# Kernel tuning notes

Hardware: AMD Instinct MI355X
Metric: run time of the kernel (lower is better)

## Reference

```python
import jax, jax.numpy as jnp
import numpy as np

B, P, V = 32, 32, 200          # batch, minPockets, vertices per pocket
NF, NT, NR, NROT = 4, 16, 5, 16
TR = NT * NR                   # 80 kernel bins
MAX_RHO = 12.0
NLIG = 7
TWO_PI = 2.0 * np.pi


def _initial_polar_grid():
    grid_rho = np.linspace(0.0, MAX_RHO, NR + 1)[1:]
    grid_theta = np.linspace(0.0, TWO_PI, NT + 1)[:-1]
    gr, gt = np.meshgrid(grid_rho, grid_theta)
    return gr.T.flatten().astype(np.float32), gt.T.flatten().astype(np.float32)


def _glorot(k, shape):
    lim = np.sqrt(6.0 / (shape[-2] + shape[-1]))
    return jax.random.uniform(k, shape, jnp.float32, -lim, lim)


def setup_inputs() -> dict:
    key = jax.random.key(0)
    ks = jax.random.split(key, 8)
    input_feat = jax.random.normal(ks[0], (B, P, V, NF), jnp.float32)
    rho_coords = jax.random.uniform(ks[1], (B, P, V, 1), jnp.float32) * MAX_RHO
    theta_coords = jax.random.uniform(ks[2], (B, P, V, 1), jnp.float32) * TWO_PI
    mask = jnp.ones((B, P, V, 1), jnp.float32)
    gr, gt = _initial_polar_grid()
    mu_rho = jnp.tile(jnp.asarray(gr)[None], (NF, 1))        # [F,TR]
    mu_theta = jnp.tile(jnp.asarray(gt)[None], (NF, 1))      # [F,TR]
    sigma_rho = jnp.full((NF, TR), MAX_RHO / 8.0, jnp.float32)
    sigma_theta = jnp.ones((NF, TR), jnp.float32)
    W_conv = _glorot(ks[3], (NF, TR, TR))
    b_conv = jnp.zeros((NF, TR), jnp.float32)
    W1 = _glorot(ks[4], (NF * TR, TR)); b1 = jnp.zeros((TR,), jnp.float32)
    W2 = _glorot(ks[5], (TR * TR, 64)); b2 = jnp.zeros((64,), jnp.float32)
    W3 = _glorot(ks[6], (64, NLIG));    b3 = jnp.zeros((NLIG,), jnp.float32)
    bn = lambda d: (jnp.ones((d,), jnp.float32), jnp.zeros((d,), jnp.float32),
                    jnp.zeros((d,), jnp.float32), jnp.ones((d,), jnp.float32))
    bn1_g, bn1_b, bn1_m, bn1_v = bn(NF * TR)
    bn2_g, bn2_b, bn2_m, bn2_v = bn(TR)
    bn3_g, bn3_b, bn3_m, bn3_v = bn(64)
    return dict(input_feat=input_feat, rho_coords=rho_coords, theta_coords=theta_coords,
                mask=mask, mu_rho=mu_rho, sigma_rho=sigma_rho, mu_theta=mu_theta,
                sigma_theta=sigma_theta, W_conv=W_conv, b_conv=b_conv, W1=W1, b1=b1,
                bn1_g=bn1_g, bn1_b=bn1_b, bn1_m=bn1_m, bn1_v=bn1_v,
                bn2_g=bn2_g, bn2_b=bn2_b, bn2_m=bn2_m, bn2_v=bn2_v,
                W2=W2, b2=b2, bn3_g=bn3_g, bn3_b=bn3_b, bn3_m=bn3_m, bn3_v=bn3_v,
                W3=W3, b3=b3)


def _bn(x, g, b, m, v, eps=1e-3):
    return (x - m) * (g * jax.lax.rsqrt(v + eps)) + b


def _conv_layer(input_feat, rho, theta, mask, mu_rho, sigma_rho, mu_theta, sigma_theta,
                W_conv, b_conv, eps=1e-5):
    # rho/theta/mask: [B,P,V,1]; mu/sigma: [F,TR]; feat: [B,P,V,F]
    # rho Gaussian is rotation-invariant -> compute once.  [B,P,V,F,TR]
    rho_g = jnp.exp(-jnp.square(rho[..., None] - mu_rho) / (jnp.square(sigma_rho) + eps))
    offs = (TWO_PI / NROT) * jnp.arange(NROT, dtype=jnp.float32)

    def step(best, off):
        th = jnp.mod(theta + off, TWO_PI)
        th_g = jnp.exp(-jnp.square(th[..., None] - mu_theta) / (jnp.square(sigma_theta) + eps))
        g = rho_g * th_g * mask[..., None]                      # [B,P,V,F,TR]
        g = g / (jnp.sum(g, axis=2, keepdims=True) + eps)       # normalize over vertices
        desc = jnp.einsum('bpvft,bpvf->bpft', g, input_feat)    # [B,P,F,TR]
        conv = jnp.einsum('bpft,ftu->bpfu', desc, W_conv) + b_conv
        return jnp.maximum(best, conv), None

    init = jnp.full((B, P, NF, TR), -jnp.inf, jnp.float32)
    best, _ = jax.lax.scan(step, init, offs)
    return best                                                  # [B,P,F,TR]


def reference(input_feat, rho_coords, theta_coords, mask, mu_rho, sigma_rho, mu_theta,
              sigma_theta, W_conv, b_conv, W1, b1, bn1_g, bn1_b, bn1_m, bn1_v,
              bn2_g, bn2_b, bn2_m, bn2_v, W2, b2, bn3_g, bn3_b, bn3_m, bn3_v, W3, b3):
    conv = _conv_layer(input_feat, rho_coords, theta_coords, mask, mu_rho, sigma_rho,
                       mu_theta, sigma_theta, W_conv, b_conv)
    x = conv.reshape(B, P, NF * TR)
    x = jax.nn.relu(_bn(x, bn1_g, bn1_b, bn1_m, bn1_v))
    x = x @ W1 + b1                                              # [B,P,TR]
    x = jax.nn.relu(_bn(x, bn2_g, bn2_b, bn2_m, bn2_v))
    cov = jnp.einsum('bpi,bpj->bij', x, x) / jnp.float32(P)      # CovarLayer [B,TR,TR]
    x = cov.reshape(B, TR * TR)
    x = jax.nn.relu(x @ W2 + b2)                                 # Dense(64, relu)
    x = _bn(x, bn3_g, bn3_b, bn3_m, bn3_v)
    return x @ W3 + b3                                           # [B, NLIG]
```

## Files before the change

### kernel.cpp

```cpp
#include <hip/hip_runtime.h>
#include <math.h>

#define B_    32
#define P_    32
#define V_    200
#define NF_   4
#define TR_   80
#define NROT_ 16
#define NLIG_ 7
#define NTH_  1024
#define PKT_  512

#define WSLOTS 33
#define CSTR   (WSLOTS * 25)
#define CTOT   (16 * CSTR)
#define RSTR   84

static constexpr float TWO_PI_F  = 6.2831854820251465f;
static constexpr float DELTA_F   = 0.39269909262657166f;

__global__ __launch_bounds__(NTH_, 4) void masif_conv_kernel(
    const float* __restrict__ feat, const float* __restrict__ rho,
    const float* __restrict__ theta, const float* __restrict__ mask,
    const float* __restrict__ mu_rho, const float* __restrict__ sigma_rho,
    const float* __restrict__ mu_theta, const float* __restrict__ sigma_theta,
    const float* __restrict__ W_conv, const float* __restrict__ b_conv,
    const float* __restrict__ W1, const float* __restrict__ b1,
    const float* __restrict__ bn1_g, const float* __restrict__ bn1_b,
    const float* __restrict__ bn1_m, const float* __restrict__ bn1_v,
    const float* __restrict__ bn2_g, const float* __restrict__ bn2_b,
    const float* __restrict__ bn2_m, const float* __restrict__ bn2_v,
    float* __restrict__ x2out)
{
    __shared__ __align__(16) float s_C[2][CTOT];
    __shared__ __align__(16) float s_V[2][V_][12];
    __shared__ float s_offs[NROT_];
    __shared__ float s_mu[5], s_isr[5];
    __shared__ float s_ist1;
    __shared__ int   s_cnt[2][16], s_start[2][17];
    __shared__ int   s_whist[2][4][16];

    const int tid = threadIdx.x;
    const int pk  = tid >> 9;
    const int lt  = tid & 511;
    const int bp  = blockIdx.x * 2 + pk;
    const size_t vb = (size_t)bp * V_;

    float* Cp = s_C[pk];

    float*  stg_th  = Cp;
    float*  stg_rho = Cp + 256;
    float*  stg_msk = Cp + 512;
    float4* stg_f4  = (float4*)(Cp + 768);

    for (int i = lt; i < V_; i += PKT_) {
        stg_th[i]  = theta[vb + i];
        stg_rho[i] = rho[vb + i];
        stg_msk[i] = mask[vb + i];
        stg_f4[i]  = ((const float4*)(feat + vb * NF_))[i];
    }
    if (tid < NROT_) s_offs[tid] = (float)tid * DELTA_F;
    if (tid < 5) {
        s_mu[tid] = mu_rho[tid * 16];
        float sg = sigma_rho[tid * 16];
        s_isr[tid] = 1.0f / (sg * sg + 1e-5f);
    }
    if (tid == 5) { float sg = sigma_theta[0]; s_ist1 = 1.0f / (sg * sg + 1e-5f); }
    if (tid >= 64 && tid < 96) ((int*)s_cnt)[tid - 64] = 0;
    __syncthreads();

    int myb = 0;
    if (lt < V_) {
        float th = stg_th[lt];
        int rs = 16;
        for (int r = 1; r < 16; ++r) {
            if (th + s_offs[r] >= TWO_PI_F) { rs = r; break; }
        }
        myb = rs - 1;
        atomicAdd(&s_cnt[pk][myb], 1);
    }

    int rkw = 0;
    {
        const unsigned long long below = (1ULL << (tid & 63)) - 1ULL;
        const int wv = lt >> 6;
        for (int b = 0; b < 16; ++b) {
            bool p = (lt < V_) && (myb == b);
            unsigned long long m = __ballot(p);
            if (p) rkw = __popcll(m & below);
            if (wv < 4 && (tid & 63) == b) s_whist[pk][wv][b] = __popcll(m);
        }
    }
    __syncthreads();
    if (lt == 0) {
        int run = 0;
        for (int k = 0; k < 16; ++k) { s_start[pk][k] = run; run += s_cnt[pk][k]; }
        s_start[pk][16] = run;
    }
    __syncthreads();

    if (lt < V_) {
        int rk = rkw;
        for (int w = 0; w < (lt >> 6); ++w) rk += s_whist[pk][w][myb];
        int pos = s_start[pk][myb] + rk;
        float th = stg_th[lt];
        float mk = stg_msk[lt];
        float4 f4 = stg_f4[lt];
        float rv = stg_rho[lt];
        float R[5];
        #pragma unroll
        for (int i = 0; i < 5; ++i) {
            float d = rv - s_mu[i];
            R[i] = __expf(-d * d * s_isr[i]);
        }
        *(float4*)&s_V[pk][pos][0] = make_float4(R[0], R[1], R[2], R[3]);
        *(float4*)&s_V[pk][pos][4] = make_float4(R[4], th, f4.x * mk, f4.y * mk);
        *(float4*)&s_V[pk][pos][8] = make_float4(f4.z * mk, f4.w * mk, mk, 0.0f);
    }
    __syncthreads();

    {
        float4 z4 = make_float4(0.f, 0.f, 0.f, 0.f);
        float4* C4 = (float4*)Cp;
        for (int e = lt; e < CTOT / 4; e += PKT_) C4[e] = z4;
    }
    __syncthreads();

    {
        const int team = lt >> 5, t32 = lt & 31;
        const int cg = t32 / 6;
        const int mq = t32 - cg * 6;
        const float ist = s_ist1;
        float acc[4][5];
        #pragma unroll
        for (int mm = 0; mm < 4; ++mm)
            #pragma unroll
            for (int i = 0; i < 5; ++i) acc[mm][i] = 0.0f;
        const int v0 = s_start[pk][team], v1 = s_start[pk][team + 1];
        const float nbase = (float)(team - 25 + mq * 4);
        if (cg < 5) {
            for (int v = v0; v < v1; ++v) {
                float4 ra = *(const float4*)&s_V[pk][v][0];
                const float r4 = s_V[pk][v][4];
                const float th = s_V[pk][v][5];
                const float ch = s_V[pk][v][6 + cg];
                float A0 = ch * ra.x, A1 = ch * ra.y, A2 = ch * ra.z,
                      A3 = ch * ra.w, A4 = ch * r4;
                #pragma unroll
                for (int mm = 0; mm < 4; ++mm) {
                    float q = fmaf(nbase + (float)mm, DELTA_F, th);
                    float w = __expf(-q * q * ist);
                    acc[mm][0] = fmaf(w, A0, acc[mm][0]);
                    acc[mm][1] = fmaf(w, A1, acc[mm][1]);
                    acc[mm][2] = fmaf(w, A2, acc[mm][2]);
                    acc[mm][3] = fmaf(w, A3, acc[mm][3]);
                    acc[mm][4] = fmaf(w, A4, acc[mm][4]);
                }
            }
            #pragma unroll
            for (int mm = 0; mm < 4; ++mm) {
                const int l = mq * 4 + mm;
                const int w = team - 1 + l;
                if (l < 20 && w >= 0 && w < WSLOTS)
                    #pragma unroll
                    for (int i = 0; i < 5; ++i)
                        Cp[team * CSTR + w * 25 + cg * 5 + i] = acc[mm][i];
            }
        }
    }
    __syncthreads();

    for (int e = lt; e < CSTR; e += PKT_) {
        float run = Cp[e];
        #pragma unroll
        for (int tk = 1; tk < 16; ++tk) {
            run += Cp[tk * CSTR + e];
            Cp[tk * CSTR + e] = run;
        }
    }
    __syncthreads();

    const float* Tb = Cp + 15 * CSTR;
    float dreg[10];
    #pragma unroll
    for (int it = 0; it < 10; ++it) {
        const int q   = lt + PKT_ * it;
        const int r   = q / 320;
        const int bin = q - r * 320;
        const int j1 = bin & 15, ci1 = bin >> 4;
        const int i1 = ci1 % 5;
        const int sD = ci1, sS = 20 + i1;
        const int wT = r - j1 + 24;
        const bool pT = (wT <= 32);
        const int wTc = pT ? wT : 32;
        const float* Tp = Tb + wTc * 25;
        float tD = Tp[sD], tS = Tp[sS];
        float D = pT ? tD : 0.0f;
        float S = pT ? tS : 0.0f;
        if (r > 0) {
            const float* Cr = Cp + (r - 1) * CSTR;
            const float* Up = Cr + wTc * 25;
            float uD = Up[sD], uS = Up[sS];
            if (pT) { D -= uD; S -= uS; }
            const int wW = wT - 16;
            const bool pW = (wW >= 0);
            const int wWc = pW ? wW : 0;
            const float* Wp = Cr + wWc * 25;
            float wD = Wp[sD], wS = Wp[sS];
            if (pW) { D += wD; S += wS; }
        }
        dreg[it] = D / (S + 1e-5f);
    }
    __syncthreads();

    float* ring    = Cp;
    float* s_pool2 = Cp + 5376;
    float* s_x1    = Cp + 6656;
    float* s_part  = Cp + 6976;

    #pragma unroll
    for (int it = 0; it < 10; ++it) {
        const int q   = lt + PKT_ * it;
        const int r   = q / 320;
        const int bin = q - r * 320;
        const int j1 = bin & 15, ci1 = bin >> 4;
        const int c1 = ci1 / 5, i1 = ci1 - c1 * 5;
        ring[r * (4 * RSTR) + c1 * RSTR + i1 * 16 + j1] = dreg[it];
    }
    __syncthreads();

    if (lt < 320) {
        const int g  = lt / 80;
        const int s  = lt - g * 80;
        const int cf = s / 20;
        const int uq = s - cf * 20;
        const int u0 = uq * 4;
        const float* Wf = W_conv + (size_t)cf * TR_ * TR_ + u0;
        const float* r0 = ring + (4 * g) * (4 * RSTR) + cf * RSTR;
        float4 a0 = make_float4(0.f, 0.f, 0.f, 0.f);
        float4 a1 = a0, a2 = a0, a3 = a0;
        #pragma unroll 4
        for (int kq = 0; kq < 20; ++kq) {
            const int k = kq * 4;
            float4 d0 = *(const float4*)&r0[k];
            float4 d1 = *(const float4*)&r0[(4 * RSTR) + k];
            float4 d2 = *(const float4*)&r0[(8 * RSTR) + k];
            float4 d3 = *(const float4*)&r0[(12 * RSTR) + k];
            float4 w0 = *(const float4*)&Wf[(size_t)(k + 0) * TR_];
            float4 w1 = *(const float4*)&Wf[(size_t)(k + 1) * TR_];
            float4 w2 = *(const float4*)&Wf[(size_t)(k + 2) * TR_];
            float4 w3 = *(const float4*)&Wf[(size_t)(k + 3) * TR_];
            a0.x = fmaf(d0.x,w0.x, fmaf(d0.y,w1.x, fmaf(d0.z,w2.x, fmaf(d0.w,w3.x, a0.x))));
            a0.y = fmaf(d0.x,w0.y, fmaf(d0.y,w1.y, fmaf(d0.z,w2.y, fmaf(d0.w,w3.y, a0.y))));
            a0.z = fmaf(d0.x,w0.z, fmaf(d0.y,w1.z, fmaf(d0.z,w2.z, fmaf(d0.w,w3.z, a0.z))));
            a0.w = fmaf(d0.x,w0.w, fmaf(d0.y,w1.w, fmaf(d0.z,w2.w, fmaf(d0.w,w3.w, a0.w))));
            a1.x = fmaf(d1.x,w0.x, fmaf(d1.y,w1.x, fmaf(d1.z,w2.x, fmaf(d1.w,w3.x, a1.x))));
            a1.y = fmaf(d1.x,w0.y, fmaf(d1.y,w1.y, fmaf(d1.z,w2.y, fmaf(d1.w,w3.y, a1.y))));
            a1.z = fmaf(d1.x,w0.z, fmaf(d1.y,w1.z, fmaf(d1.z,w2.z, fmaf(d1.w,w3.z, a1.z))));
            a1.w = fmaf(d1.x,w0.w, fmaf(d1.y,w1.w, fmaf(d1.z,w2.w, fmaf(d1.w,w3.w, a1.w))));
            a2.x = fmaf(d2.x,w0.x, fmaf(d2.y,w1.x, fmaf(d2.z,w2.x, fmaf(d2.w,w3.x, a2.x))));
            a2.y = fmaf(d2.x,w0.y, fmaf(d2.y,w1.y, fmaf(d2.z,w2.y, fmaf(d2.w,w3.y, a2.y))));
            a2.z = fmaf(d2.x,w0.z, fmaf(d2.y,w1.z, fmaf(d2.z,w2.z, fmaf(d2.w,w3.z, a2.z))));
            a2.w = fmaf(d2.x,w0.w, fmaf(d2.y,w1.w, fmaf(d2.z,w2.w, fmaf(d2.w,w3.w, a2.w))));
            a3.x = fmaf(d3.x,w0.x, fmaf(d3.y,w1.x, fmaf(d3.z,w2.x, fmaf(d3.w,w3.x, a3.x))));
            a3.y = fmaf(d3.x,w0.y, fmaf(d3.y,w1.y, fmaf(d3.z,w2.y, fmaf(d3.w,w3.y, a3.y))));
            a3.z = fmaf(d3.x,w0.z, fmaf(d3.y,w1.z, fmaf(d3.z,w2.z, fmaf(d3.w,w3.z, a3.z))));
            a3.w = fmaf(d3.x,w0.w, fmaf(d3.y,w1.w, fmaf(d3.z,w2.w, fmaf(d3.w,w3.w, a3.w))));
        }
        float4 m;
        m.x = fmaxf(fmaxf(a0.x, a1.x), fmaxf(a2.x, a3.x));
        m.y = fmaxf(fmaxf(a0.y, a1.y), fmaxf(a2.y, a3.y));
        m.z = fmaxf(fmaxf(a0.z, a1.z), fmaxf(a2.z, a3.z));
        m.w = fmaxf(fmaxf(a0.w, a1.w), fmaxf(a2.w, a3.w));
        *(float4*)&s_pool2[g * 320 + cf * TR_ + u0] = m;
    }
    __syncthreads();

    if (lt < 320) {
        float best = fmaxf(fmaxf(s_pool2[lt], s_pool2[320 + lt]),
                           fmaxf(s_pool2[640 + lt], s_pool2[960 + lt]));
        best += b_conv[lt];
        float x1 = (best - bn1_m[lt]) * (bn1_g[lt] * rsqrtf(bn1_v[lt] + 1e-3f))
                   + bn1_b[lt];
        s_x1[lt] = fmaxf(x1, 0.0f);
    }
    __syncthreads();
    for (int q = lt; q < 640; q += PKT_) {
        const int c = q / TR_;
        const int ue = q - c * TR_;
        float p = 0.0f;
        const int i0 = c * 40;
        #pragma unroll 8
        for (int i = i0; i < i0 + 40; ++i)
            p = fmaf(s_x1[i], W1[(size_t)i * TR_ + ue], p);
        s_part[q] = p;
    }
    __syncthreads();
    if (lt < TR_) {
        float h = b1[lt];
        #pragma unroll
        for (int c = 0; c < 8; ++c) h += s_part[c * TR_ + lt];
        float x2 = (h - bn2_m[lt]) * (bn2_g[lt] * rsqrtf(bn2_v[lt] + 1e-3f))
                   + bn2_b[lt];
        x2out[(size_t)bp * TR_ + lt] = fmaxf(x2, 0.0f);
    }
}

__global__ __launch_bounds__(256) void masif_head_partial(
    const float* __restrict__ x2,
    const float* __restrict__ W2,
    float* __restrict__ hpart)
{
    __shared__ __align__(16) float s_x[P_ * TR_];
    __shared__ __align__(16) float s_cov[10 * TR_];
    __shared__ float s_red[4][64];

    const int tid = threadIdx.x;
    const int b = blockIdx.x >> 3, c = blockIdx.x & 7;

    for (int i = tid; i < P_ * TR_; i += 256)
        s_x[i] = x2[(size_t)b * P_ * TR_ + i];
    __syncthreads();

    for (int o = tid; o < 800; o += 256) {
        int il = o / TR_, j = o - il * TR_;
        int i = c * 10 + il;
        float s = 0.0f;
        #pragma unroll 4
        for (int p = 0; p < P_; ++p)
            s = fmaf(s_x[p * TR_ + i], s_x[p * TR_ + j], s);
        s_cov[o] = s * (1.0f / (float)P_);
    }
    __syncthreads();

    {
        const int o = tid & 63, sub = tid >> 6;
        float acc = 0.0f;
        const int q0 = sub * 200;
        const size_t gbase = (size_t)(c * 800) * 64 + o;
        #pragma unroll 8
        for (int q = q0; q < q0 + 200; ++q)
            acc = fmaf(s_cov[q], W2[gbase + (size_t)q * 64], acc);
        s_red[sub][o] = acc;
    }
    __syncthreads();
    if (tid < 64)
        hpart[(size_t)b * 512 + c * 64 + tid] =
            s_red[0][tid] + s_red[1][tid] + s_red[2][tid] + s_red[3][tid];
}

__global__ __launch_bounds__(64) void masif_head_final(
    const float* __restrict__ hpart,
    const float* __restrict__ b2,
    const float* __restrict__ bn3_g, const float* __restrict__ bn3_b,
    const float* __restrict__ bn3_m, const float* __restrict__ bn3_v,
    const float* __restrict__ W3, const float* __restrict__ b3,
    float* __restrict__ out)
{
    __shared__ float s_h[64];
    const int tid = threadIdx.x;
    const int b = blockIdx.x;

    float h = b2[tid];
    #pragma unroll
    for (int c = 0; c < 8; ++c) h += hpart[(size_t)b * 512 + c * 64 + tid];
    h = fmaxf(h, 0.0f);
    s_h[tid] = (h - bn3_m[tid]) * (bn3_g[tid] * rsqrtf(bn3_v[tid] + 1e-3f))
               + bn3_b[tid];
    __syncthreads();

    if (tid < NLIG_) {
        float y = b3[tid];
        #pragma unroll
        for (int k = 0; k < 64; ++k)
            y = fmaf(s_h[k], W3[k * NLIG_ + tid], y);
        out[b * NLIG_ + tid] = y;
    }
}

extern "C" void kernel_launch(void* const* d_in, const int* in_sizes, int n_in,
                              void* d_out, int out_size, void* d_ws, size_t ws_size,
                              hipStream_t stream)
{
    const float* feat      = (const float*)d_in[0];
    const float* rho       = (const float*)d_in[1];
    const float* theta     = (const float*)d_in[2];
    const float* mask      = (const float*)d_in[3];
    const float* mu_rho    = (const float*)d_in[4];
    const float* sigma_rho = (const float*)d_in[5];
    const float* mu_theta  = (const float*)d_in[6];
    const float* sigma_th  = (const float*)d_in[7];
    const float* W_conv    = (const float*)d_in[8];
    const float* b_conv    = (const float*)d_in[9];
    const float* W1        = (const float*)d_in[10];
    const float* b1        = (const float*)d_in[11];
    const float* bn1_g     = (const float*)d_in[12];
    const float* bn1_b     = (const float*)d_in[13];
    const float* bn1_m     = (const float*)d_in[14];
    const float* bn1_v     = (const float*)d_in[15];
    const float* bn2_g     = (const float*)d_in[16];
    const float* bn2_b     = (const float*)d_in[17];
    const float* bn2_m     = (const float*)d_in[18];
    const float* bn2_v     = (const float*)d_in[19];
    const float* W2        = (const float*)d_in[20];
    const float* b2        = (const float*)d_in[21];
    const float* bn3_g     = (const float*)d_in[22];
    const float* bn3_b     = (const float*)d_in[23];
    const float* bn3_m     = (const float*)d_in[24];
    const float* bn3_v     = (const float*)d_in[25];
    const float* W3        = (const float*)d_in[26];
    const float* b3        = (const float*)d_in[27];

    float* x2ws  = (float*)d_ws;
    float* hpart = (float*)d_ws + (size_t)B_ * P_ * TR_;

    masif_conv_kernel<<<dim3(B_ * P_ / 2), dim3(NTH_), 0, stream>>>(
        feat, rho, theta, mask, mu_rho, sigma_rho, mu_theta, sigma_th,
        W_conv, b_conv, W1, b1,
        bn1_g, bn1_b, bn1_m, bn1_v, bn2_g, bn2_b, bn2_m, bn2_v, x2ws);

    masif_head_partial<<<dim3(B_ * 8), dim3(256), 0, stream>>>(x2ws, W2, hpart);

    masif_head_final<<<dim3(B_), dim3(64), 0, stream>>>(
        hpart, b2, bn3_g, bn3_b, bn3_m, bn3_v, W3, b3, (float*)d_out);
}
```

Measured before the change: 67.84 us.

## Restructure polar-bin accumulation so each lane owns one rotation slot

The accumulation stage is remapped so each lane handles one rotation window slot and accumulates all 25 channel-by-rho products, computing one exp per vertex instead of four per lane across channel groups. Staging buffers move to their own shared array, which lets the C-buffer zeroing overlap with the vertex scatter and drops one barrier. The prefix-sum pass is vectorised to float2 with a padded stride, and the shared rotation-offset table is replaced by inline arithmetic. The cost is fewer active lanes (20 of 32) with 25 accumulators each, which raises register pressure, and extra shared memory for staging may reduce occupancy.

```diff
diff --git a/kernel.cpp b/kernel.cpp
--- a/kernel.cpp
+++ b/kernel.cpp
@@ -12,7 +12,7 @@
 #define PKT_  512
 
 #define WSLOTS 33
-#define CSTR   (WSLOTS * 25)
+#define CSTR   828
 #define CTOT   (16 * CSTR)
 #define RSTR   84
 
@@ -34,7 +34,7 @@
 {
     __shared__ __align__(16) float s_C[2][CTOT];
     __shared__ __align__(16) float s_V[2][V_][12];
-    __shared__ float s_offs[NROT_];
+    __shared__ __align__(16) float s_stg[2][1408];
     __shared__ float s_mu[5], s_isr[5];
     __shared__ float s_ist1;
     __shared__ int   s_cnt[2][16], s_start[2][17];
@@ -48,10 +48,10 @@
 
     float* Cp = s_C[pk];
 
-    float*  stg_th  = Cp;
-    float*  stg_rho = Cp + 256;
-    float*  stg_msk = Cp + 512;
-    float4* stg_f4  = (float4*)(Cp + 768);
+    float*  stg_th  = s_stg[pk];
+    float*  stg_rho = s_stg[pk] + 200;
+    float*  stg_msk = s_stg[pk] + 400;
+    float4* stg_f4  = (float4*)(s_stg[pk] + 608);
 
     for (int i = lt; i < V_; i += PKT_) {
         stg_th[i]  = theta[vb + i];
@@ -59,7 +59,6 @@
         stg_msk[i] = mask[vb + i];
         stg_f4[i]  = ((const float4*)(feat + vb * NF_))[i];
     }
-    if (tid < NROT_) s_offs[tid] = (float)tid * DELTA_F;
     if (tid < 5) {
         s_mu[tid] = mu_rho[tid * 16];
         float sg = sigma_rho[tid * 16];
@@ -74,7 +73,7 @@
         float th = stg_th[lt];
         int rs = 16;
         for (int r = 1; r < 16; ++r) {
-            if (th + s_offs[r] >= TWO_PI_F) { rs = r; break; }
+            if (th + (float)r * DELTA_F >= TWO_PI_F) { rs = r; break; }
         }
         myb = rs - 1;
         atomicAdd(&s_cnt[pk][myb], 1);
@@ -99,6 +98,11 @@
     }
     __syncthreads();
 
+    {
+        float4 z4 = make_float4(0.f, 0.f, 0.f, 0.f);
+        float4* C4 = (float4*)Cp;
+        for (int e = lt; e < CTOT / 4; e += PKT_) C4[e] = z4;
+    }
     if (lt < V_) {
         int rk = rkw;
         for (int w = 0; w < (lt >> 6); ++w) rk += s_whist[pk][w][myb];
@@ -120,62 +124,48 @@
     __syncthreads();
 
     {
-        float4 z4 = make_float4(0.f, 0.f, 0.f, 0.f);
-        float4* C4 = (float4*)Cp;
-        for (int e = lt; e < CTOT / 4; e += PKT_) C4[e] = z4;
-    }
-    __syncthreads();
-
-    {
         const int team = lt >> 5, t32 = lt & 31;
-        const int cg = t32 / 6;
-        const int mq = t32 - cg * 6;
-        const float ist = s_ist1;
-        float acc[4][5];
-        #pragma unroll
-        for (int mm = 0; mm < 4; ++mm)
+        const int w = team - 1 + t32;
+        if (t32 < 20 && w >= 0 && w < WSLOTS) {
+            const float ist = s_ist1;
+            const float nf = (float)(team - 25 + t32);
+            const int v0 = s_start[pk][team], v1 = s_start[pk][team + 1];
+            float acc[25];
             #pragma unroll
-            for (int i = 0; i < 5; ++i) acc[mm][i] = 0.0f;
-        const int v0 = s_start[pk][team], v1 = s_start[pk][team + 1];
-        const float nbase = (float)(team - 25 + mq * 4);
-        if (cg < 5) {
+            for (int i = 0; i < 25; ++i) acc[i] = 0.0f;
             for (int v = v0; v < v1; ++v) {
                 float4 ra = *(const float4*)&s_V[pk][v][0];
-                const float r4 = s_V[pk][v][4];
-                const float th = s_V[pk][v][5];
-                const float ch = s_V[pk][v][6 + cg];
-                float A0 = ch * ra.x, A1 = ch * ra.y, A2 = ch * ra.z,
-                      A3 = ch * ra.w, A4 = ch * r4;
+                float4 rb = *(const float4*)&s_V[pk][v][4];
+                float4 rc = *(const float4*)&s_V[pk][v][8];
+                float q  = fmaf(nf, DELTA_F, rb.y);
+                float wg = __expf(-q * q * ist);
+                float R[5]  = {ra.x, ra.y, ra.z, ra.w, rb.x};
+                float ch[5] = {rb.z, rb.w, rc.x, rc.y, rc.z};
                 #pragma unroll
-                for (int mm = 0; mm < 4; ++mm) {
-                    float q = fmaf(nbase + (float)mm, DELTA_F, th);
-                    float w = __expf(-q * q * ist);
-                    acc[mm][0] = fmaf(w, A0, acc[mm][0]);
-                    acc[mm][1] = fmaf(w, A1, acc[mm][1]);
-                    acc[mm][2] = fmaf(w, A2, acc[mm][2]);
-                    acc[mm][3] = fmaf(w, A3, acc[mm][3]);
-                    acc[mm][4] = fmaf(w, A4, acc[mm][4]);
+                for (int c = 0; c < 5; ++c) {
+                    float t = wg * ch[c];
+                    #pragma unroll
+                    for (int i = 0; i < 5; ++i)
+                        acc[c * 5 + i] = fmaf(t, R[i], acc[c * 5 + i]);
                 }
             }
+            float* dst = Cp + team * CSTR + w * 25;
             #pragma unroll
-            for (int mm = 0; mm < 4; ++mm) {
-                const int l = mq * 4 + mm;
-                const int w = team - 1 + l;
-                if (l < 20 && w >= 0 && w < WSLOTS)
-                    #pragma unroll
-                    for (int i = 0; i < 5; ++i)
-                        Cp[team * CSTR + w * 25 + cg * 5 + i] = acc[mm][i];
+            for (int i = 0; i < 25; ++i) dst[i] = acc[i];
+        }
+    }
+    __syncthreads();
+
+    {
+        float2* C2 = (float2*)Cp;
+        for (int e = lt; e < CSTR / 2; e += PKT_) {
+            float2 run = C2[e];
+            #pragma unroll
+            for (int tk = 1; tk < 16; ++tk) {
+                float2 g = C2[tk * (CSTR / 2) + e];
+                run.x += g.x; run.y += g.y;
+                C2[tk * (CSTR / 2) + e] = run;
             }
-        }
-    }
-    __syncthreads();
-
-    for (int e = lt; e < CSTR; e += PKT_) {
-        float run = Cp[e];
-        #pragma unroll
-        for (int tk = 1; tk < 16; ++tk) {
-            run += Cp[tk * CSTR + e];
-            Cp[tk * CSTR + e] = run;
         }
     }
     __syncthreads();
```

Result: faster. 63.47 us (-6.4%).
